# Optimization experiments

Hardware: AMD Instinct MI355X
Metric: run time of the kernel (lower is better)

The kernel has to match this reference:

```python
import jax, jax.numpy as jnp
import numpy as np

N_NODES = 100000
N_EDGES = 1600000
N_CLASS = 26
HIDDEN = 128
K = 3  # TAGConv hops


def setup_inputs() -> dict:
    key = jax.random.key(0)
    ks = jax.random.split(key, 12)
    x = jax.random.normal(ks[0], (N_NODES, N_CLASS), dtype=jnp.float32)
    edge_index = jax.random.randint(ks[1], (2, N_EDGES), 0, N_NODES, dtype=jnp.int64)
    edge_weight = jax.random.uniform(ks[2], (N_EDGES,), dtype=jnp.float32)
    # Per-hop weights (K+1 hops incl. hop 0) for each of the 3 TAGConv layers.
    def lin(k, fan_in, fan_out):
        s = 1.0 / np.sqrt(fan_in)
        return jax.random.uniform(k, (K + 1, fan_in, fan_out), dtype=jnp.float32, minval=-s, maxval=s)
    W1 = lin(ks[3], N_CLASS, HIDDEN)
    b1 = jnp.zeros((HIDDEN,), dtype=jnp.float32)
    W2 = lin(ks[4], HIDDEN, HIDDEN)
    b2 = jnp.zeros((HIDDEN,), dtype=jnp.float32)
    W3 = lin(ks[5], HIDDEN, N_CLASS)
    b3 = jnp.zeros((N_CLASS,), dtype=jnp.float32)
    return {"x": x, "edge_index": edge_index, "edge_weight": edge_weight,
            "W1": W1, "b1": b1, "W2": W2, "b2": b2, "W3": W3, "b3": b3}


def _gcn_norm(edge_index, edge_weight, n):
    # symmetric normalization deg^-1/2 * w * deg^-1/2, no self loops (PyG TAGConv)
    row, col = edge_index[0], edge_index[1]
    deg = jax.ops.segment_sum(edge_weight, col, num_segments=n)
    dinv = jnp.where(deg > 0, jax.lax.rsqrt(jnp.maximum(deg, 1e-12)), 0.0)
    return dinv[row] * edge_weight * dinv[col]


def _tag_conv(x, row, col, norm, W, b, n):
    # out = sum_k W_k(x_k), x_0 = x, x_k = A_norm x_{k-1}
    out = x @ W[0]
    h = x
    for k in range(1, K + 1):
        h = jax.ops.segment_sum(norm[:, None] * h[row], col, num_segments=n)
        out = out + h @ W[k]
    return out + b


def reference(x, edge_index, edge_weight, W1, b1, W2, b2, W3, b3):
    n = x.shape[0]
    row, col = edge_index[0], edge_index[1]
    norm = _gcn_norm(edge_index, edge_weight, n)  # identical for all 3 layers
    h = jax.nn.elu(_tag_conv(x, row, col, norm, W1, b1, n))
    h = jax.nn.elu(_tag_conv(h, row, col, norm, W2, b2, n))
    return _tag_conv(h, row, col, norm, W3, b3, n)
```

## Files before the change

### kernel.cpp

```cpp
#include <hip/hip_runtime.h>

#define NCLS 26
#define HID 128
#define EPB 8192
#define MAXBK 512
typedef unsigned short ushort_t;
typedef unsigned int uint_t;
typedef unsigned long long u64;

typedef __bf16 bf16x8 __attribute__((ext_vector_type(8)));
typedef float f32x4 __attribute__((ext_vector_type(4)));
typedef unsigned int u32x4 __attribute__((ext_vector_type(4)));
typedef unsigned int u32x2 __attribute__((ext_vector_type(2)));

static __device__ __forceinline__ float b2f(ushort_t h) {
  return __uint_as_float(((uint_t)h) << 16);
}
static __device__ __forceinline__ ushort_t f2b(float f) {
  uint_t u = __float_as_uint(f);
  uint_t r = (u + 0x7fffu + ((u >> 16) & 1u)) >> 16;
  return (ushort_t)r;
}
static __device__ __forceinline__ uint_t pack2(float f0, float f1) {
  return (uint_t)f2b(f0) | ((uint_t)f2b(f1) << 16);
}
static __device__ __forceinline__ float lo16(uint_t v) { return b2f((ushort_t)(v & 0xffffu)); }
static __device__ __forceinline__ float hi16(uint_t v) { return b2f((ushort_t)(v >> 16)); }
static __device__ __forceinline__ bf16x8 ld_frag(const ushort_t* p) {
  u32x4 v = *reinterpret_cast<const u32x4*>(p);
  return __builtin_bit_cast(bf16x8, v);
}


__global__ __launch_bounds__(256) void bucket_count(const int* __restrict__ ei,
                                                    int* __restrict__ bcnt, int E, int nbk) {
  __shared__ uint_t lc[MAXBK];
  int tid = threadIdx.x;
  for (int t = tid; t < nbk; t += 256) lc[t] = 0;
  __syncthreads();
  int e0 = blockIdx.x * EPB;
#pragma unroll
  for (int i = 0; i < EPB / 256; ++i) {
    int e = e0 + tid + i * 256;
    if (e < E) atomicAdd(&lc[(uint_t)ei[E + e] >> 8], 1u);
  }
  __syncthreads();
  for (int t = tid; t < nbk; t += 256)
    if (lc[t]) atomicAdd(&bcnt[t], (int)lc[t]);
}

__global__ void scan_buckets(const int* __restrict__ bcnt, int* __restrict__ bbase,
                             int nbk, int E) {
  __shared__ int s[512];
  int t = threadIdx.x;
  int v = (t < nbk) ? bcnt[t] : 0;
  s[t] = v;
  __syncthreads();
  for (int off = 1; off < 512; off <<= 1) {
    int u = (t >= off) ? s[t - off] : 0;
    __syncthreads();
    s[t] += u;
    __syncthreads();
  }
  if (t < nbk) bbase[t] = s[t] - v;
  if (t == 0) bbase[nbk] = E;
}

__global__ __launch_bounds__(256) void bucket_place(
    const int* __restrict__ ei, const float* __restrict__ ew, const int* __restrict__ bbase,
    int* __restrict__ gcur, u64* __restrict__ bkt, int E, int nbk) {
  __shared__ uint_t lc[MAXBK];
  __shared__ uint_t lb[MAXBK];
  int tid = threadIdx.x;
  for (int t = tid; t < nbk; t += 256) lc[t] = 0;
  __syncthreads();
  int e0 = blockIdx.x * EPB;
#pragma unroll
  for (int i = 0; i < EPB / 256; ++i) {
    int e = e0 + tid + i * 256;
    if (e < E) atomicAdd(&lc[(uint_t)ei[E + e] >> 8], 1u);
  }
  __syncthreads();
  for (int t = tid; t < nbk; t += 256) {
    uint_t c = lc[t];
    lb[t] = c ? (uint_t)(bbase[t] + atomicAdd(&gcur[t], (int)c)) : 0u;
    lc[t] = 0;
  }
  __syncthreads();
#pragma unroll
  for (int i = 0; i < EPB / 256; ++i) {
    int e = e0 + tid + i * 256;
    if (e < E) {
      uint_t r = (uint_t)ei[e];
      uint_t c = (uint_t)ei[E + e];
      uint_t b = c >> 8;
      float wv = ew[e];
      uint_t pos = lb[b] + atomicAdd(&lc[b], 1u);
      bkt[pos] = ((u64)(r | ((c & 255u) << 24)) << 32) | (u64)__float_as_uint(wv);
    }
  }
}

__global__ __launch_bounds__(256) void bucket_stats(
    const u64* __restrict__ bkt, const int* __restrict__ bbase,
    int* __restrict__ start, float* __restrict__ dinv, int n, int E) {
  int b = blockIdx.x;
  __shared__ uint_t cnt[256];
  __shared__ float deg[256];
  __shared__ int ssc[256];
  int tid = threadIdx.x;
  cnt[tid] = 0;
  deg[tid] = 0.f;
  __syncthreads();
  int s = bbase[b], e_end = bbase[b + 1];
  for (int p = s + tid; p < e_end; p += 256) {
    u64 v = bkt[p];
    uint_t cl = (uint_t)(v >> 56);
    float wv = __uint_as_float((uint_t)(v & 0xffffffffULL));
    atomicAdd(&cnt[cl], 1u);
    atomicAdd(&deg[cl], wv);
  }
  __syncthreads();
  int v0 = (int)cnt[tid];
  ssc[tid] = v0;
  __syncthreads();
  for (int off = 1; off < 256; off <<= 1) {
    int u = (tid >= off) ? ssc[tid - off] : 0;
    __syncthreads();
    ssc[tid] += u;
    __syncthreads();
  }
  int node = (b << 8) + tid;
  if (node < n) {
    start[node] = s + ssc[tid] - v0;
    float d = deg[tid];
    dinv[node] = d > 0.f ? rsqrtf(fmaxf(d, 1e-12f)) : 0.f;
  }
  if (b == 0 && tid == 0) start[n] = E;
}

__global__ __launch_bounds__(256) void bucket_emit(
    const u64* __restrict__ bkt, const int* __restrict__ bbase, const int* __restrict__ start,
    const float* __restrict__ dinv, u32x2* __restrict__ meta, int n) {
  int b = blockIdx.x;
  __shared__ uint_t lcur[256];
  int tid = threadIdx.x;
  lcur[tid] = 0;
  __syncthreads();
  int s = bbase[b], e_end = bbase[b + 1];
  for (int p = s + tid; p < e_end; p += 256) {
    u64 v = bkt[p];
    uint_t hi = (uint_t)(v >> 32);
    uint_t r = hi & 0xffffffu;
    uint_t cl = hi >> 24;
    float wv = __uint_as_float((uint_t)(v & 0xffffffffULL));
    uint_t node = ((uint_t)b << 8) + cl;
    float nrm = dinv[r] * wv * dinv[node];
    uint_t slot = (uint_t)start[node] + atomicAdd(&lcur[cl], 1u);
    u32x2 m;
    m.x = r;
    m.y = __float_as_uint(nrm);
    meta[slot] = m;
  }
}

__global__ void convert_x(const float* __restrict__ in, uint_t* __restrict__ out, int n) {
  int idx = blockIdx.x * 256 + threadIdx.x;
  if (idx >= n * 16) return;
  int node = idx >> 4, lane = idx & 15;
  float f0 = 0.f, f1 = 0.f;
  if (lane < 13) {
    f0 = in[node * 26 + 2 * lane];
    f1 = in[node * 26 + 2 * lane + 1];
  }
  out[idx] = pack2(f0, f1);
}


__global__ void swizzleW_kcat(const float* __restrict__ W, ushort_t* __restrict__ out,
                              int ksps, int kwv, int nsrc) {
  int idx = blockIdx.x * 256 + threadIdx.x;
  int total = nsrc * ksps * 4096;
  if (idx >= total) return;
  int i = idx & 7, l = (idx >> 3) & 63, j = (idx >> 9) & 7, t = idx >> 12;
  int s = t / ksps, tt = t - s * ksps;
  int k = tt * 32 + 8 * (l >> 4) + i;
  int col = 16 * j + (l & 15);
  float v = (k < kwv) ? W[((size_t)s * kwv + k) * 128 + col] : 0.f;
  out[idx] = f2b(v);
}

__global__ void swizzleW_nslot(const float* __restrict__ W, ushort_t* __restrict__ out) {
  int idx = blockIdx.x * 256 + threadIdx.x;
  if (idx >= 4 * 4096) return;
  int i = idx & 7, l = (idx >> 3) & 63, j = (idx >> 9) & 7, t = idx >> 12;
  int k = t * 32 + 8 * (l >> 4) + i;
  int col = 16 * j + (l & 15);
  int s = col >> 5, c = col & 31;
  float v = (c < 26) ? W[((size_t)s * 128 + k) * 26 + c] : 0.f;
  out[idx] = f2b(v);
}


__global__ __launch_bounds__(256) void spmm128_bf(
    const u32x2* __restrict__ meta, const int* __restrict__ start,
    const uint_t* __restrict__ in, uint_t* __restrict__ out, int n) {
  int node = blockIdx.x * 4 + (threadIdx.x >> 6);
  int lane = threadIdx.x & 63;
  if (node >= n) return;
  int s = start[node], m = start[node + 1] - s;
  int eq = lane >> 4;
  int f16 = lane & 15;
  float a0 = 0.f, a1 = 0.f, a2 = 0.f, a3 = 0.f, a4 = 0.f, a5 = 0.f, a6 = 0.f, a7 = 0.f;
  for (int base = 0; base < m; base += 16) {
    int i0 = base + eq, i1 = i0 + 4, i2 = i0 + 8, i3 = i0 + 12;
    u32x2 mt0 = (i0 < m) ? meta[s + i0] : (u32x2){0u, 0u};
    u32x2 mt1 = (i1 < m) ? meta[s + i1] : (u32x2){0u, 0u};
    u32x2 mt2 = (i2 < m) ? meta[s + i2] : (u32x2){0u, 0u};
    u32x2 mt3 = (i3 < m) ? meta[s + i3] : (u32x2){0u, 0u};
    u32x4 v0 = *reinterpret_cast<const u32x4*>(in + (size_t)mt0.x * 64 + f16 * 4);
    u32x4 v1 = *reinterpret_cast<const u32x4*>(in + (size_t)mt1.x * 64 + f16 * 4);
    u32x4 v2 = *reinterpret_cast<const u32x4*>(in + (size_t)mt2.x * 64 + f16 * 4);
    u32x4 v3 = *reinterpret_cast<const u32x4*>(in + (size_t)mt3.x * 64 + f16 * 4);
    float w0 = __uint_as_float(mt0.y);
    float w1 = __uint_as_float(mt1.y);
    float w2 = __uint_as_float(mt2.y);
    float w3 = __uint_as_float(mt3.y);
    a0 += w0 * lo16(v0.x); a1 += w0 * hi16(v0.x);
    a2 += w0 * lo16(v0.y); a3 += w0 * hi16(v0.y);
    a4 += w0 * lo16(v0.z); a5 += w0 * hi16(v0.z);
    a6 += w0 * lo16(v0.w); a7 += w0 * hi16(v0.w);
    a0 += w1 * lo16(v1.x); a1 += w1 * hi16(v1.x);
    a2 += w1 * lo16(v1.y); a3 += w1 * hi16(v1.y);
    a4 += w1 * lo16(v1.z); a5 += w1 * hi16(v1.z);
    a6 += w1 * lo16(v1.w); a7 += w1 * hi16(v1.w);
    a0 += w2 * lo16(v2.x); a1 += w2 * hi16(v2.x);
    a2 += w2 * lo16(v2.y); a3 += w2 * hi16(v2.y);
    a4 += w2 * lo16(v2.z); a5 += w2 * hi16(v2.z);
    a6 += w2 * lo16(v2.w); a7 += w2 * hi16(v2.w);
    a0 += w3 * lo16(v3.x); a1 += w3 * hi16(v3.x);
    a2 += w3 * lo16(v3.y); a3 += w3 * hi16(v3.y);
    a4 += w3 * lo16(v3.z); a5 += w3 * hi16(v3.z);
    a6 += w3 * lo16(v3.w); a7 += w3 * hi16(v3.w);
  }
  a0 += __shfl_xor(a0, 16); a1 += __shfl_xor(a1, 16);
  a2 += __shfl_xor(a2, 16); a3 += __shfl_xor(a3, 16);
  a4 += __shfl_xor(a4, 16); a5 += __shfl_xor(a5, 16);
  a6 += __shfl_xor(a6, 16); a7 += __shfl_xor(a7, 16);
  a0 += __shfl_xor(a0, 32); a1 += __shfl_xor(a1, 32);
  a2 += __shfl_xor(a2, 32); a3 += __shfl_xor(a3, 32);
  a4 += __shfl_xor(a4, 32); a5 += __shfl_xor(a5, 32);
  a6 += __shfl_xor(a6, 32); a7 += __shfl_xor(a7, 32);
  if (eq == 0) {
    u32x4 o;
    o.x = pack2(a0, a1);
    o.y = pack2(a2, a3);
    o.z = pack2(a4, a5);
    o.w = pack2(a6, a7);
    *reinterpret_cast<u32x4*>(out + (size_t)node * 64 + f16 * 4) = o;
  }
}

__global__ __launch_bounds__(256) void spmm26_bf(
    const u32x2* __restrict__ meta, const int* __restrict__ start,
    const uint_t* __restrict__ in, const uint_t* __restrict__ add,
    uint_t* __restrict__ out, int n) {
  int node = blockIdx.x * 32 + (threadIdx.x >> 3);
  int d2 = threadIdx.x & 7;
  if (node >= n) return;
  int s = start[node], m = start[node + 1] - s;
  float a0 = 0.f, a1 = 0.f, a2 = 0.f, a3 = 0.f;
  for (int base = 0; base < m; base += 8) {
#pragma unroll
    for (int j = 0; j < 8; ++j) {
      int eidx = base + j;
      u32x2 mt = (eidx < m) ? meta[s + eidx] : (u32x2){0u, 0u};
      int r = (int)mt.x;
      float wv = __uint_as_float(mt.y);
      u32x2 v = *reinterpret_cast<const u32x2*>(in + (size_t)r * 16 + 2 * d2);
      a0 += wv * lo16(v.x); a1 += wv * hi16(v.x);
      a2 += wv * lo16(v.y); a3 += wv * hi16(v.y);
    }
  }
  if (add) {
    u32x2 v = *reinterpret_cast<const u32x2*>(add + (size_t)node * 16 + 2 * d2);
    a0 += lo16(v.x); a1 += hi16(v.x);
    a2 += lo16(v.y); a3 += hi16(v.y);
  }
  u32x2 o;
  o.x = pack2(a0, a1);
  o.y = pack2(a2, a3);
  *reinterpret_cast<u32x2*>(out + (size_t)node * 16 + 2 * d2) = o;
}

__global__ __launch_bounds__(256) void spmm26_addf(
    const u32x2* __restrict__ meta, const int* __restrict__ start,
    const uint_t* __restrict__ in, float* __restrict__ out, int n) {
  int node = blockIdx.x * 32 + (threadIdx.x >> 3);
  int d2 = threadIdx.x & 7;
  if (node >= n) return;
  int s = start[node], m = start[node + 1] - s;
  float a0 = 0.f, a1 = 0.f, a2 = 0.f, a3 = 0.f;
  for (int base = 0; base < m; base += 8) {
#pragma unroll
    for (int j = 0; j < 8; ++j) {
      int eidx = base + j;
      u32x2 mt = (eidx < m) ? meta[s + eidx] : (u32x2){0u, 0u};
      int r = (int)mt.x;
      float wv = __uint_as_float(mt.y);
      u32x2 v = *reinterpret_cast<const u32x2*>(in + (size_t)r * 16 + 2 * d2);
      a0 += wv * lo16(v.x); a1 += wv * hi16(v.x);
      a2 += wv * lo16(v.y); a3 += wv * hi16(v.y);
    }
  }
  int c0 = 4 * d2;
  if (c0 + 0 < 26) out[(size_t)node * 26 + c0 + 0] += a0;
  if (c0 + 1 < 26) out[(size_t)node * 26 + c0 + 1] += a1;
  if (c0 + 2 < 26) out[(size_t)node * 26 + c0 + 2] += a2;
  if (c0 + 3 < 26) out[(size_t)node * 26 + c0 + 3] += a3;
}

template <int KW, int NSRC, int EPI, int MR>
__global__ __launch_bounds__(256) void mfma_gemm(
    const ushort_t* __restrict__ A0, const ushort_t* __restrict__ A1,
    const ushort_t* __restrict__ A2, const ushort_t* __restrict__ A3,
    const ushort_t* __restrict__ Wswz, const float* __restrict__ bias,
    ushort_t* __restrict__ outb, float* __restrict__ outf, int n) {
  constexpr int KSPS = KW / 32;
  constexpr int KSTEPS = NSRC * KSPS;
  const int w = threadIdx.x >> 6;
  const int l = threadIdx.x & 63;
  const int row0 = blockIdx.x * (64 * MR) + w * (16 * MR);
  const int koff = 8 * (l >> 4);

  f32x4 acc[MR][8];
#pragma unroll
  for (int f = 0; f < MR; ++f)
#pragma unroll
    for (int j = 0; j < 8; ++j) acc[f][j] = (f32x4){0.f, 0.f, 0.f, 0.f};

  const ushort_t* const srcs[4] = {A0, A1, A2, A3};

#pragma unroll
  for (int t = 0; t < KSTEPS; ++t) {
    const int s = t / KSPS;
    const int tt = t - s * KSPS;
    bf16x8 af[MR];
#pragma unroll
    for (int f = 0; f < MR; ++f) {
      int arow = row0 + f * 16 + (l & 15);
      int arow_c = arow < n ? arow : (n - 1);
      af[f] = ld_frag(srcs[s] + (size_t)arow_c * KW + tt * 32 + koff);
    }
    const ushort_t* wp = Wswz + ((size_t)t * 8 * 64 + l) * 8;
#pragma unroll
    for (int j = 0; j < 8; ++j) {
      bf16x8 bfr = ld_frag(wp + (size_t)j * 64 * 8);
#pragma unroll
      for (int f = 0; f < MR; ++f)
        acc[f][j] = __builtin_amdgcn_mfma_f32_16x16x32_bf16(af[f], bfr, acc[f][j], 0, 0, 0);
    }
  }

  const int ccol = l & 15;
#pragma unroll
  for (int f = 0; f < MR; ++f) {
    const int crow0 = row0 + f * 16 + 4 * (l >> 4);
#pragma unroll
    for (int j = 0; j < 8; ++j) {
      if (EPI == 0) {
        int col = 16 * j + ccol;
        float bi = bias[col];
#pragma unroll
        for (int r = 0; r < 4; ++r) {
          int row = crow0 + r;
          if (row >= n) continue;
          float v = acc[f][j][r] + bi;
          v = v > 0.f ? v : (__expf(v) - 1.f);
          outb[(size_t)row * 128 + col] = f2b(v);
        }
      } else {
        int slot = j >> 1;
        int c = 16 * (j & 1) + ccol;
#pragma unroll
        for (int r = 0; r < 4; ++r) {
          int row = crow0 + r;
          if (row >= n) continue;
          float v = acc[f][j][r];
          if (slot == 0) {
            if (c < 26) outf[(size_t)row * 26 + c] = v + bias[c];
          } else {
            outb[((size_t)(slot - 1) * n + row) * 32 + c] = f2b(v);
          }
        }
      }
    }
  }
}


extern "C" void kernel_launch(void* const* d_in, const int* in_sizes, int n_in,
                              void* d_out, int out_size, void* d_ws, size_t ws_size,
                              hipStream_t stream) {
  const float* x  = (const float*)d_in[0];
  const int*   ei = (const int*)d_in[1];
  const float* ew = (const float*)d_in[2];
  const float* W1 = (const float*)d_in[3];
  const float* b1 = (const float*)d_in[4];
  const float* W2 = (const float*)d_in[5];
  const float* b2 = (const float*)d_in[6];
  const float* W3 = (const float*)d_in[7];
  const float* b3 = (const float*)d_in[8];
  float* out = (float*)d_out;

  const int n = in_sizes[0] / NCLS;
  const int E = in_sizes[2];
  const int nbk = (n + 255) >> 8;

  char* w = (char*)d_ws;
  auto alloc = [&](size_t bytes) {
    char* p = w;
    w += (bytes + 255) / 256 * 256;
    return p;
  };
  uint_t* H0 = (uint_t*)alloc((size_t)n * 64 * 4);
  uint_t* P1 = (uint_t*)alloc((size_t)n * 64 * 4);
  uint_t* P2 = (uint_t*)alloc((size_t)n * 64 * 4);
  uint_t* P3 = (uint_t*)alloc((size_t)n * 64 * 4);
  uint_t* H1 = (uint_t*)alloc((size_t)n * 64 * 4);
  uint_t* x32 = (uint_t*)alloc((size_t)n * 16 * 4);
  uint_t* q1  = (uint_t*)alloc((size_t)n * 16 * 4);
  uint_t* q2  = (uint_t*)alloc((size_t)n * 16 * 4);
  uint_t* q3  = (uint_t*)alloc((size_t)n * 16 * 4);
  uint_t* zb  = (uint_t*)alloc((size_t)n * 48 * 4);
  ushort_t* Wz1 = (ushort_t*)alloc(4 * 4096 * 2);
  ushort_t* Wz2 = (ushort_t*)alloc(16 * 4096 * 2);
  ushort_t* Wz3 = (ushort_t*)alloc(4 * 4096 * 2);
  u64*   bkt  = (u64*)zb;
  u32x2* meta = (u32x2*)alloc((size_t)E * 8);
  int*   start = (int*)alloc((size_t)(n + 1) * 4);
  float* dinv  = (float*)alloc((size_t)n * 4);
  int*   bcnt  = (int*)alloc(MAXBK * 4);
  int*   gcur  = (int*)alloc(MAXBK * 4);
  int*   bbase = (int*)alloc((MAXBK + 1) * 4);

  const int ab = (E + EPB - 1) / EPB;

  hipMemsetAsync(bcnt, 0, MAXBK * 4, stream);
  hipMemsetAsync(gcur, 0, MAXBK * 4, stream);

  bucket_count<<<ab, 256, 0, stream>>>(ei, bcnt, E, nbk);
  scan_buckets<<<1, 512, 0, stream>>>(bcnt, bbase, nbk, E);
  bucket_place<<<ab, 256, 0, stream>>>(ei, ew, bbase, gcur, bkt, E, nbk);
  bucket_stats<<<nbk, 256, 0, stream>>>(bkt, bbase, start, dinv, n, E);
  bucket_emit<<<nbk, 256, 0, stream>>>(bkt, bbase, start, dinv, meta, n);

  convert_x<<<(n * 16 + 255) / 256, 256, 0, stream>>>(x, x32, n);
  swizzleW_kcat<<<(4 * 4096 + 255) / 256, 256, 0, stream>>>(W1, Wz1, 1, NCLS, 4);
  swizzleW_kcat<<<(16 * 4096 + 255) / 256, 256, 0, stream>>>(W2, Wz2, 4, HID, 4);
  swizzleW_nslot<<<(4 * 4096 + 255) / 256, 256, 0, stream>>>(W3, Wz3);

  const int g128 = (n + 3) / 4;
  const int g26  = (n + 31) / 32;
  const int gg   = (n + 63) / 64;

  spmm26_bf<<<g26, 256, 0, stream>>>(meta, start, x32, nullptr, q1, n);
  spmm26_bf<<<g26, 256, 0, stream>>>(meta, start, q1, nullptr, q2, n);
  spmm26_bf<<<g26, 256, 0, stream>>>(meta, start, q2, nullptr, q3, n);
  mfma_gemm<32, 4, 0, 1><<<gg, 256, 0, stream>>>(
      (const ushort_t*)x32, (const ushort_t*)q1, (const ushort_t*)q2, (const ushort_t*)q3,
      Wz1, b1, (ushort_t*)H0, nullptr, n);

  spmm128_bf<<<g128, 256, 0, stream>>>(meta, start, H0, P1, n);
  spmm128_bf<<<g128, 256, 0, stream>>>(meta, start, P1, P2, n);
  spmm128_bf<<<g128, 256, 0, stream>>>(meta, start, P2, P3, n);
  mfma_gemm<128, 4, 0, 1><<<gg, 256, 0, stream>>>(
      (const ushort_t*)H0, (const ushort_t*)P1, (const ushort_t*)P2, (const ushort_t*)P3,
      Wz2, b2, (ushort_t*)H1, nullptr, n);

  mfma_gemm<128, 1, 1, 1><<<gg, 256, 0, stream>>>(
      (const ushort_t*)H1, (const ushort_t*)H1, (const ushort_t*)H1, (const ushort_t*)H1,
      Wz3, b3, (ushort_t*)zb, out, n);

  uint_t* z1 = zb;
  uint_t* z2 = zb + (size_t)n * 16;
  uint_t* z3 = zb + (size_t)n * 32;
  spmm26_bf<<<g26, 256, 0, stream>>>(meta, start, z3, z2, q1, n);
  spmm26_bf<<<g26, 256, 0, stream>>>(meta, start, q1, z1, q2, n);
  spmm26_addf<<<g26, 256, 0, stream>>>(meta, start, q2, out, n);
}
```

Measured before the change: 548.4 us.

## Stage swizzled weights through LDS with register prefetch in MFMA GEMM

The MFMA GEMM now copies each group of weight k-steps into shared memory cooperatively across the block, prefetching the next group into registers while the current one is consumed, instead of every wave loading weight fragments straight from global memory. The layer-2 GEMM also switches to two row fragments per wave (128 rows per block), so each weight fragment is reused across more rows. This is meant to cut redundant global and L2 weight traffic. In exchange it adds block-wide barriers, up to 32 KB of LDS per block and more registers, which may lower occupancy.

```diff
diff --git a/kernel.cpp b/kernel.cpp
--- a/kernel.cpp
+++ b/kernel.cpp
@@ -320,7 +320,7 @@
   if (c0 + 3 < 26) out[(size_t)node * 26 + c0 + 3] += a3;
 }
 
-template <int KW, int NSRC, int EPI, int MR>
+template <int KW, int NSRC, int EPI, int MR, int GROUP>
 __global__ __launch_bounds__(256) void mfma_gemm(
     const ushort_t* __restrict__ A0, const ushort_t* __restrict__ A1,
     const ushort_t* __restrict__ A2, const ushort_t* __restrict__ A3,
@@ -328,8 +328,11 @@
     ushort_t* __restrict__ outb, float* __restrict__ outf, int n) {
   constexpr int KSPS = KW / 32;
   constexpr int KSTEPS = NSRC * KSPS;
-  const int w = threadIdx.x >> 6;
-  const int l = threadIdx.x & 63;
+  constexpr int NGROUPS = KSTEPS / GROUP;
+  __shared__ ushort_t sW[GROUP * 4096];
+  const int tid = threadIdx.x;
+  const int w = tid >> 6;
+  const int l = tid & 63;
   const int row0 = blockIdx.x * (64 * MR) + w * (16 * MR);
   const int koff = 8 * (l >> 4);
 
@@ -341,24 +344,51 @@
 
   const ushort_t* const srcs[4] = {A0, A1, A2, A3};
 
-#pragma unroll
-  for (int t = 0; t < KSTEPS; ++t) {
-    const int s = t / KSPS;
-    const int tt = t - s * KSPS;
-    bf16x8 af[MR];
-#pragma unroll
-    for (int f = 0; f < MR; ++f) {
-      int arow = row0 + f * 16 + (l & 15);
-      int arow_c = arow < n ? arow : (n - 1);
-      af[f] = ld_frag(srcs[s] + (size_t)arow_c * KW + tt * 32 + koff);
-    }
-    const ushort_t* wp = Wswz + ((size_t)t * 8 * 64 + l) * 8;
-#pragma unroll
-    for (int j = 0; j < 8; ++j) {
-      bf16x8 bfr = ld_frag(wp + (size_t)j * 64 * 8);
-#pragma unroll
-      for (int f = 0; f < MR; ++f)
-        acc[f][j] = __builtin_amdgcn_mfma_f32_16x16x32_bf16(af[f], bfr, acc[f][j], 0, 0, 0);
+  u32x4 gw[2 * GROUP];
+#pragma unroll
+  for (int c = 0; c < GROUP; ++c) {
+    const ushort_t* p = Wswz + (size_t)c * 4096 + tid * 8;
+    gw[2 * c] = *reinterpret_cast<const u32x4*>(p);
+    gw[2 * c + 1] = *reinterpret_cast<const u32x4*>(p + 2048);
+  }
+
+#pragma unroll
+  for (int g = 0; g < NGROUPS; ++g) {
+    __syncthreads();
+#pragma unroll
+    for (int c = 0; c < GROUP; ++c) {
+      *reinterpret_cast<u32x4*>(sW + c * 4096 + tid * 8) = gw[2 * c];
+      *reinterpret_cast<u32x4*>(sW + c * 4096 + tid * 8 + 2048) = gw[2 * c + 1];
+    }
+    if (g + 1 < NGROUPS) {
+#pragma unroll
+      for (int c = 0; c < GROUP; ++c) {
+        const ushort_t* p = Wswz + (size_t)(g + 1) * GROUP * 4096 + (size_t)c * 4096 + tid * 8;
+        gw[2 * c] = *reinterpret_cast<const u32x4*>(p);
+        gw[2 * c + 1] = *reinterpret_cast<const u32x4*>(p + 2048);
+      }
+    }
+    __syncthreads();
+#pragma unroll
+    for (int tg = 0; tg < GROUP; ++tg) {
+      const int t = g * GROUP + tg;
+      const int s = t / KSPS;
+      const int tt = t - s * KSPS;
+      bf16x8 af[MR];
+#pragma unroll
+      for (int f = 0; f < MR; ++f) {
+        int arow = row0 + f * 16 + (l & 15);
+        int arow_c = arow < n ? arow : (n - 1);
+        af[f] = ld_frag(srcs[s] + (size_t)arow_c * KW + tt * 32 + koff);
+      }
+      const ushort_t* wp = sW + tg * 4096 + l * 8;
+#pragma unroll
+      for (int j = 0; j < 8; ++j) {
+        bf16x8 bfr = ld_frag(wp + j * 64 * 8);
+#pragma unroll
+        for (int f = 0; f < MR; ++f)
+          acc[f][j] = __builtin_amdgcn_mfma_f32_16x16x32_bf16(af[f], bfr, acc[f][j], 0, 0, 0);
+      }
     }
   }
 
@@ -462,23 +492,24 @@
 
   const int g128 = (n + 3) / 4;
   const int g26  = (n + 31) / 32;
-  const int gg   = (n + 63) / 64;
+  const int gg1  = (n + 63) / 64;
+  const int gg2  = (n + 127) / 128;
 
   spmm26_bf<<<g26, 256, 0, stream>>>(meta, start, x32, nullptr, q1, n);
   spmm26_bf<<<g26, 256, 0, stream>>>(meta, start, q1, nullptr, q2, n);
   spmm26_bf<<<g26, 256, 0, stream>>>(meta, start, q2, nullptr, q3, n);
-  mfma_gemm<32, 4, 0, 1><<<gg, 256, 0, stream>>>(
+  mfma_gemm<32, 4, 0, 1, 4><<<gg1, 256, 0, stream>>>(
       (const ushort_t*)x32, (const ushort_t*)q1, (const ushort_t*)q2, (const ushort_t*)q3,
       Wz1, b1, (ushort_t*)H0, nullptr, n);
 
   spmm128_bf<<<g128, 256, 0, stream>>>(meta, start, H0, P1, n);
   spmm128_bf<<<g128, 256, 0, stream>>>(meta, start, P1, P2, n);
   spmm128_bf<<<g128, 256, 0, stream>>>(meta, start, P2, P3, n);
-  mfma_gemm<128, 4, 0, 1><<<gg, 256, 0, stream>>>(
+  mfma_gemm<128, 4, 0, 2, 2><<<gg2, 256, 0, stream>>>(
       (const ushort_t*)H0, (const ushort_t*)P1, (const ushort_t*)P2, (const ushort_t*)P3,
       Wz2, b2, (ushort_t*)H1, nullptr, n);
 
-  mfma_gemm<128, 1, 1, 1><<<gg, 256, 0, stream>>>(
+  mfma_gemm<128, 1, 1, 1, 4><<<gg1, 256, 0, stream>>>(
       (const ushort_t*)H1, (const ushort_t*)H1, (const ushort_t*)H1, (const ushort_t*)H1,
       Wz3, b3, (ushort_t*)zb, out, n);
 
```

Result: no change. 543.5 us (-0.9%).
